# Performance work log

Measured on AMD Instinct MI355X. Metric: run time of the kernel, lower is better.

Reference implementation:

```python
import jax, jax.numpy as jnp
import numpy as np

N_NODES = 40000
N_EDGES = 640000
IN_CH = 128
HID_CH = 128
BN_EPS = 1e-5


def setup_inputs() -> dict:
    key = jax.random.key(0)
    k_x, k_ei, k_w, k_g = jax.random.split(key, 4)
    x = jax.random.normal(k_x, (N_NODES, IN_CH), dtype=jnp.float32)
    edge_index = jax.random.randint(k_ei, (2, N_EDGES), 0, N_NODES, dtype=jnp.int32)
    # Glorot init for GCNConv weight, zero bias (PyG defaults)
    limit = float(np.sqrt(6.0 / (IN_CH + HID_CH)))
    W = jax.random.uniform(k_w, (IN_CH, HID_CH), dtype=jnp.float32, minval=-limit, maxval=limit)
    b = jnp.zeros((HID_CH,), dtype=jnp.float32)
    gamma = jnp.ones((HID_CH,), dtype=jnp.float32)
    beta = jnp.zeros((HID_CH,), dtype=jnp.float32)
    return {"x": x, "edge_index": edge_index, "W": W, "b": b, "gamma": gamma, "beta": beta}


def reference(x, edge_index, W, b, gamma, beta):
    N = x.shape[0]
    src, dst = edge_index[0], edge_index[1]

    # --- GCNConv: h = x @ W, symmetric-normalized aggregation with self-loops ---
    h = x @ W  # [N, H]
    ones = jnp.ones((src.shape[0],), dtype=x.dtype)
    deg = jax.ops.segment_sum(ones, dst, num_segments=N) + 1.0  # +1 for self-loop
    dinv = jax.lax.rsqrt(deg)  # deg >= 1 always
    norm = dinv[src] * dinv[dst]  # [E]
    msg = h[src] * norm[:, None]  # [E, H] gather
    agg = jax.ops.segment_sum(msg, dst, num_segments=N)  # scatter-add
    agg = agg + h * (dinv * dinv)[:, None]  # self-loop contribution
    out = agg + b  # bias added after aggregation (PyG GCNConv)

    # --- BatchNorm1d (training mode: batch stats, biased variance) ---
    mean = jnp.mean(out, axis=0)
    var = jnp.mean((out - mean) ** 2, axis=0)
    out = gamma * (out - mean) * jax.lax.rsqrt(var + BN_EPS) + beta

    # --- ReLU (dropout is a no-op in eval) ---
    return jax.nn.relu(out)
```

## Files before the change

kernel.cpp:

```cpp
#include <hip/hip_runtime.h>

#define N_NODES 40000
#define N_EDGES 640000
#define CH 128
#define BN_EPS 1e-5f
#define CAP 64
#define MM_ROWS 32
#define MM_BLOCKS (N_NODES / MM_ROWS)
#define FILL_BLOCKS ((N_EDGES + 255) / 256)


__device__ __forceinline__ float bf_lo(unsigned u) { return __uint_as_float(u << 16); }
__device__ __forceinline__ float bf_hi(unsigned u) { return __uint_as_float(u & 0xffff0000u); }
__device__ __forceinline__ unsigned short f2bf(float f) {
    unsigned u = __float_as_uint(f);
    unsigned r = 0x7fffu + ((u >> 16) & 1u);
    return (unsigned short)((u + r) >> 16);
}
__device__ __forceinline__ unsigned pack2bf(float a, float b) {
    return (unsigned)f2bf(a) | ((unsigned)f2bf(b) << 16);
}

__global__ __launch_bounds__(256) void mm_fill_kernel(const float* __restrict__ x,
                                                      const float* __restrict__ W,
                                                      unsigned short* __restrict__ hbf,
                                                      const int* __restrict__ src,
                                                      const int* __restrict__ dst,
                                                      int* __restrict__ cnt,
                                                      unsigned short* __restrict__ bucket16) {
    __shared__ unsigned Wsb[CH * CH / 2];
    __shared__ unsigned xsb[CH * 16];
    int t = threadIdx.x;
    int bb = blockIdx.x;
    if (bb % 3 != 0) {
        int fillIdx = bb - (bb / 3) - 1;
        int base = cnt[N_NODES];
        int e = fillIdx * 256 + t;
        if (e < N_EDGES) {
            int d = dst[e];
            int slot = atomicAdd(&cnt[d], 1) - base;
            if (slot < CAP) bucket16[d * CAP + slot] = (unsigned short)src[e];
        }
        return;
    }
    int mmIdx = bb / 3;
    for (int i = t; i < CH * CH / 4; i += 256) {
        float4 w = ((const float4*)W)[i];
        uint2 p;
        p.x = pack2bf(w.x, w.y);
        p.y = pack2bf(w.z, w.w);
        ((uint2*)Wsb)[i] = p;
    }
    size_t row0 = (size_t)mmIdx * MM_ROWS;
    {
        int p = t >> 4;
        int k4a = t & 15;
#pragma unroll
        for (int kk = 0; kk < 2; ++kk) {
            int k4 = k4a + kk * 16;
            float4 xa = ((const float4*)(x + (row0 + p) * CH))[k4];
            float4 xb = ((const float4*)(x + (row0 + p + 16) * CH))[k4];
            xsb[(k4 * 4 + 0) * 16 + p] = pack2bf(xa.x, xb.x);
            xsb[(k4 * 4 + 1) * 16 + p] = pack2bf(xa.y, xb.y);
            xsb[(k4 * 4 + 2) * 16 + p] = pack2bf(xa.z, xb.z);
            xsb[(k4 * 4 + 3) * 16 + p] = pack2bf(xa.w, xb.w);
        }
    }
    __syncthreads();
    int ch4 = t & 31;
    int rg = t >> 5;
    float4 accA = {0,0,0,0}, accB = {0,0,0,0}, accC = {0,0,0,0}, accD = {0,0,0,0};
#pragma unroll 8
    for (int k = 0; k < CH; ++k) {
        uint2 wp = ((const uint2*)Wsb)[k * 32 + ch4];
        unsigned xpa = xsb[k * 16 + rg];
        unsigned xpb = xsb[k * 16 + rg + 8];
        float w0 = bf_lo(wp.x), w1 = bf_hi(wp.x), w2 = bf_lo(wp.y), w3 = bf_hi(wp.y);
        float xa0 = bf_lo(xpa), xa1 = bf_hi(xpa);
        float xb0 = bf_lo(xpb), xb1 = bf_hi(xpb);
        accA.x += xa0 * w0; accA.y += xa0 * w1; accA.z += xa0 * w2; accA.w += xa0 * w3;
        accB.x += xa1 * w0; accB.y += xa1 * w1; accB.z += xa1 * w2; accB.w += xa1 * w3;
        accC.x += xb0 * w0; accC.y += xb0 * w1; accC.z += xb0 * w2; accC.w += xb0 * w3;
        accD.x += xb1 * w0; accD.y += xb1 * w1; accD.z += xb1 * w2; accD.w += xb1 * w3;
    }
    uint2 o;
    o.x = pack2bf(accA.x, accA.y); o.y = pack2bf(accA.z, accA.w);
    ((uint2*)(hbf + (row0 + rg) * CH))[ch4] = o;
    o.x = pack2bf(accB.x, accB.y); o.y = pack2bf(accB.z, accB.w);
    ((uint2*)(hbf + (row0 + rg + 16) * CH))[ch4] = o;
    o.x = pack2bf(accC.x, accC.y); o.y = pack2bf(accC.z, accC.w);
    ((uint2*)(hbf + (row0 + rg + 8) * CH))[ch4] = o;
    o.x = pack2bf(accD.x, accD.y); o.y = pack2bf(accD.z, accD.w);
    ((uint2*)(hbf + (row0 + rg + 24) * CH))[ch4] = o;
}

__global__ __launch_bounds__(256) void aggregate_kernel(const unsigned short* __restrict__ bucket16,
                                                        const int* __restrict__ cnt,
                                                        const unsigned short* __restrict__ hbf,
                                                        const float* __restrict__ b,
                                                        float* __restrict__ out,
                                                        float* __restrict__ sums32) {
    __shared__ float bsum[CH], bsq[CH];
    int t = threadIdx.x;
    if (t < CH) { bsum[t] = 0.0f; bsq[t] = 0.0f; }
    __syncthreads();
    int base = cnt[N_NODES];
    int n = blockIdx.x * 4 + (t >> 6);
    int lane = t & 63;
    int quarter = lane >> 4;
    int ql = lane & 15;
    int cn = cnt[n] - base;
    int m = cn < CAP ? cn : CAP;
    float dn = rsqrtf((float)cn + 1.0f);
    const uint4* h4 = (const uint4*)hbf;
    unsigned sx_pre = (lane < m) ? (unsigned)bucket16[n * CAP + lane] : 0u;
    float a0 = 0, a1 = 0, a2 = 0, a3 = 0, a4 = 0, a5 = 0, a6 = 0, a7 = 0;
    for (int jj = 0; jj < m; jj += 16) {
        int e = jj + quarter * 4;
        unsigned sx0 = (unsigned)__shfl((int)sx_pre, e, 64);
        unsigned sx1 = (unsigned)__shfl((int)sx_pre, e + 1, 64);
        unsigned sx2 = (unsigned)__shfl((int)sx_pre, e + 2, 64);
        unsigned sx3 = (unsigned)__shfl((int)sx_pre, e + 3, 64);
        int c0g = cnt[sx0];
        int c1g = cnt[sx1];
        int c2g = cnt[sx2];
        int c3g = cnt[sx3];
        uint4 r0 = h4[(size_t)sx0 * 16 + ql];
        uint4 r1 = h4[(size_t)sx1 * 16 + ql];
        uint4 r2 = h4[(size_t)sx2 * 16 + ql];
        uint4 r3 = h4[(size_t)sx3 * 16 + ql];
        float d0 = (e     < m) ? rsqrtf((float)(c0g - base) + 1.0f) : 0.0f;
        float d1 = (e + 1 < m) ? rsqrtf((float)(c1g - base) + 1.0f) : 0.0f;
        float d2 = (e + 2 < m) ? rsqrtf((float)(c2g - base) + 1.0f) : 0.0f;
        float d3 = (e + 3 < m) ? rsqrtf((float)(c3g - base) + 1.0f) : 0.0f;
        a0 += bf_lo(r0.x) * d0; a1 += bf_hi(r0.x) * d0;
        a2 += bf_lo(r0.y) * d0; a3 += bf_hi(r0.y) * d0;
        a4 += bf_lo(r0.z) * d0; a5 += bf_hi(r0.z) * d0;
        a6 += bf_lo(r0.w) * d0; a7 += bf_hi(r0.w) * d0;
        a0 += bf_lo(r1.x) * d1; a1 += bf_hi(r1.x) * d1;
        a2 += bf_lo(r1.y) * d1; a3 += bf_hi(r1.y) * d1;
        a4 += bf_lo(r1.z) * d1; a5 += bf_hi(r1.z) * d1;
        a6 += bf_lo(r1.w) * d1; a7 += bf_hi(r1.w) * d1;
        a0 += bf_lo(r2.x) * d2; a1 += bf_hi(r2.x) * d2;
        a2 += bf_lo(r2.y) * d2; a3 += bf_hi(r2.y) * d2;
        a4 += bf_lo(r2.z) * d2; a5 += bf_hi(r2.z) * d2;
        a6 += bf_lo(r2.w) * d2; a7 += bf_hi(r2.w) * d2;
        a0 += bf_lo(r3.x) * d3; a1 += bf_hi(r3.x) * d3;
        a2 += bf_lo(r3.y) * d3; a3 += bf_hi(r3.y) * d3;
        a4 += bf_lo(r3.z) * d3; a5 += bf_hi(r3.z) * d3;
        a6 += bf_lo(r3.w) * d3; a7 += bf_hi(r3.w) * d3;
    }
    a0 += __shfl_xor(a0, 16, 64); a0 += __shfl_xor(a0, 32, 64);
    a1 += __shfl_xor(a1, 16, 64); a1 += __shfl_xor(a1, 32, 64);
    a2 += __shfl_xor(a2, 16, 64); a2 += __shfl_xor(a2, 32, 64);
    a3 += __shfl_xor(a3, 16, 64); a3 += __shfl_xor(a3, 32, 64);
    a4 += __shfl_xor(a4, 16, 64); a4 += __shfl_xor(a4, 32, 64);
    a5 += __shfl_xor(a5, 16, 64); a5 += __shfl_xor(a5, 32, 64);
    a6 += __shfl_xor(a6, 16, 64); a6 += __shfl_xor(a6, 32, 64);
    a7 += __shfl_xor(a7, 16, 64); a7 += __shfl_xor(a7, 32, 64);
    if (quarter == 0) {
        uint4 raw = h4[(size_t)n * 16 + ql];
        float s2 = dn * dn;
        float4 bv0 = ((const float4*)b)[ql * 2];
        float4 bv1 = ((const float4*)b)[ql * 2 + 1];
        float o0 = a0 * dn + bf_lo(raw.x) * s2 + bv0.x;
        float o1 = a1 * dn + bf_hi(raw.x) * s2 + bv0.y;
        float o2 = a2 * dn + bf_lo(raw.y) * s2 + bv0.z;
        float o3 = a3 * dn + bf_hi(raw.y) * s2 + bv0.w;
        float o4 = a4 * dn + bf_lo(raw.z) * s2 + bv1.x;
        float o5 = a5 * dn + bf_hi(raw.z) * s2 + bv1.y;
        float o6 = a6 * dn + bf_lo(raw.w) * s2 + bv1.z;
        float o7 = a7 * dn + bf_hi(raw.w) * s2 + bv1.w;
        float4* op = (float4*)(out + (size_t)n * CH + ql * 8);
        float4 w0 = {o0, o1, o2, o3};
        float4 w1 = {o4, o5, o6, o7};
        op[0] = w0;
        op[1] = w1;
        int c0 = ql * 8;
        atomicAdd(&bsum[c0 + 0], o0); atomicAdd(&bsq[c0 + 0], o0 * o0);
        atomicAdd(&bsum[c0 + 1], o1); atomicAdd(&bsq[c0 + 1], o1 * o1);
        atomicAdd(&bsum[c0 + 2], o2); atomicAdd(&bsq[c0 + 2], o2 * o2);
        atomicAdd(&bsum[c0 + 3], o3); atomicAdd(&bsq[c0 + 3], o3 * o3);
        atomicAdd(&bsum[c0 + 4], o4); atomicAdd(&bsq[c0 + 4], o4 * o4);
        atomicAdd(&bsum[c0 + 5], o5); atomicAdd(&bsq[c0 + 5], o5 * o5);
        atomicAdd(&bsum[c0 + 6], o6); atomicAdd(&bsq[c0 + 6], o6 * o6);
        atomicAdd(&bsum[c0 + 7], o7); atomicAdd(&bsq[c0 + 7], o7 * o7);
    }
    __syncthreads();
    atomicAdd(&sums32[(blockIdx.x & 31) * 256 + t], (t < CH) ? bsum[t] : bsq[t - CH]);
}

__global__ __launch_bounds__(256) void bn_relu_kernel(float* __restrict__ out,
                                                      const float* __restrict__ sums32,
                                                      const float* __restrict__ gamma,
                                                      const float* __restrict__ beta) {
    __shared__ float sc[CH], sh[CH];
    int t = threadIdx.x;
    if (t < CH) {
        float P = sums32[32 * 256];
        float s = -32.0f * P, q = -32.0f * P;
#pragma unroll
        for (int k = 0; k < 32; ++k) {
            s += sums32[k * 256 + t];
            q += sums32[k * 256 + CH + t];
        }
        const float invN = 1.0f / (float)N_NODES;
        float mean = s * invN;
        float var = q * invN - mean * mean;
        float scale = gamma[t] * rsqrtf(var + BN_EPS);
        sc[t] = scale;
        sh[t] = beta[t] - mean * scale;
    }
    __syncthreads();
    int i = blockIdx.x * 256 + t;
    int c0 = (i & 31) * 4;
    float4 v = ((float4*)out)[i];
    float r0 = v.x * sc[c0] + sh[c0];
    float r1 = v.y * sc[c0 + 1] + sh[c0 + 1];
    float r2 = v.z * sc[c0 + 2] + sh[c0 + 2];
    float r3 = v.w * sc[c0 + 3] + sh[c0 + 3];
    v.x = r0 > 0.0f ? r0 : 0.0f;
    v.y = r1 > 0.0f ? r1 : 0.0f;
    v.z = r2 > 0.0f ? r2 : 0.0f;
    v.w = r3 > 0.0f ? r3 : 0.0f;
    ((float4*)out)[i] = v;
}

extern "C" void kernel_launch(void* const* d_in, const int* in_sizes, int n_in,
                              void* d_out, int out_size, void* d_ws, size_t ws_size,
                              hipStream_t stream) {
    const float* x = (const float*)d_in[0];
    const int* ei = (const int*)d_in[1];
    const float* W = (const float*)d_in[2];
    const float* b = (const float*)d_in[3];
    const float* gamma = (const float*)d_in[4];
    const float* beta = (const float*)d_in[5];
    float* out = (float*)d_out;
    const int* src = ei;
    const int* dst = ei + N_EDGES;
    char* ws = (char*)d_ws;

    unsigned short* hbf = (unsigned short*)ws;
    int* cnt = (int*)(ws + 10240000);
    float* sums32 = (float*)(ws + 10400256);
    unsigned short* bucket16 = (unsigned short*)(ws + 10433280);

    mm_fill_kernel<<<MM_BLOCKS + FILL_BLOCKS, 256, 0, stream>>>(x, W, hbf, src, dst, cnt,
                                                                bucket16);
    aggregate_kernel<<<N_NODES / 4, 256, 0, stream>>>(bucket16, cnt, hbf, b, out, sums32);
    bn_relu_kernel<<<N_NODES * CH / 4 / 256, 256, 0, stream>>>(out, sums32, gamma, beta);
}
```

Before: 196.0 us.

## Use bf16 MFMA for the x@W matmul and rebalance fused fill blocks

Replaces the scalar FMA loop in the fused matmul/fill kernel with 16x16x32 bf16 MFMA instructions. W is transposed into padded shared memory and each block now handles 16 rows instead of 32. Fill blocks each process two edges, which changes the interleaving ratio of fill to matmul blocks. This moves the GEMM onto matrix cores to cut ALU time, but each block re-stages all of W for fewer rows. The transposed W store also writes scalar shorts with a strided pattern, which may cause LDS bank conflicts.

New measurement: 201.8 us. 3.0% more time.

```diff
diff --git a/kernel.cpp b/kernel.cpp
--- a/kernel.cpp
+++ b/kernel.cpp
@@ -5,10 +5,14 @@
 #define CH 128
 #define BN_EPS 1e-5f
 #define CAP 64
-#define MM_ROWS 32
+#define MM_ROWS 16
 #define MM_BLOCKS (N_NODES / MM_ROWS)
-#define FILL_BLOCKS ((N_EDGES + 255) / 256)
-
+#define FILL_BLOCKS (N_EDGES / 512)
+#define XPAD 136
+
+
+typedef short short8 __attribute__((ext_vector_type(8)));
+typedef float f32x4 __attribute__((ext_vector_type(4)));
 
 __device__ __forceinline__ float bf_lo(unsigned u) { return __uint_as_float(u << 16); }
 __device__ __forceinline__ float bf_hi(unsigned u) { return __uint_as_float(u & 0xffff0000u); }
@@ -28,70 +32,63 @@
                                                       const int* __restrict__ dst,
                                                       int* __restrict__ cnt,
                                                       unsigned short* __restrict__ bucket16) {
-    __shared__ unsigned Wsb[CH * CH / 2];
-    __shared__ unsigned xsb[CH * 16];
+    __shared__ unsigned short Wt[CH * XPAD];
+    __shared__ unsigned short xs[MM_ROWS * XPAD];
     int t = threadIdx.x;
     int bb = blockIdx.x;
-    if (bb % 3 != 0) {
-        int fillIdx = bb - (bb / 3) - 1;
+    if (bb % 3 == 0) {
+        int fillIdx = bb / 3;
         int base = cnt[N_NODES];
-        int e = fillIdx * 256 + t;
-        if (e < N_EDGES) {
-            int d = dst[e];
-            int slot = atomicAdd(&cnt[d], 1) - base;
-            if (slot < CAP) bucket16[d * CAP + slot] = (unsigned short)src[e];
-        }
+        int e0 = fillIdx * 512 + t;
+        int e1 = e0 + 256;
+        int d0 = dst[e0], d1 = dst[e1];
+        int s0 = src[e0], s1 = src[e1];
+        int slot0 = atomicAdd(&cnt[d0], 1) - base;
+        int slot1 = atomicAdd(&cnt[d1], 1) - base;
+        if (slot0 < CAP) bucket16[d0 * CAP + slot0] = (unsigned short)s0;
+        if (slot1 < CAP) bucket16[d1 * CAP + slot1] = (unsigned short)s1;
         return;
     }
-    int mmIdx = bb / 3;
+    int mmIdx = bb - (bb / 3) - 1;
+    size_t row0 = (size_t)mmIdx * MM_ROWS;
     for (int i = t; i < CH * CH / 4; i += 256) {
         float4 w = ((const float4*)W)[i];
-        uint2 p;
-        p.x = pack2bf(w.x, w.y);
-        p.y = pack2bf(w.z, w.w);
-        ((uint2*)Wsb)[i] = p;
-    }
-    size_t row0 = (size_t)mmIdx * MM_ROWS;
-    {
-        int p = t >> 4;
-        int k4a = t & 15;
-#pragma unroll
-        for (int kk = 0; kk < 2; ++kk) {
-            int k4 = k4a + kk * 16;
-            float4 xa = ((const float4*)(x + (row0 + p) * CH))[k4];
-            float4 xb = ((const float4*)(x + (row0 + p + 16) * CH))[k4];
-            xsb[(k4 * 4 + 0) * 16 + p] = pack2bf(xa.x, xb.x);
-            xsb[(k4 * 4 + 1) * 16 + p] = pack2bf(xa.y, xb.y);
-            xsb[(k4 * 4 + 2) * 16 + p] = pack2bf(xa.z, xb.z);
-            xsb[(k4 * 4 + 3) * 16 + p] = pack2bf(xa.w, xb.w);
+        int k = i >> 5;
+        int c0 = (i & 31) * 4;
+        Wt[(c0 + 0) * XPAD + k] = f2bf(w.x);
+        Wt[(c0 + 1) * XPAD + k] = f2bf(w.y);
+        Wt[(c0 + 2) * XPAD + k] = f2bf(w.z);
+        Wt[(c0 + 3) * XPAD + k] = f2bf(w.w);
+    }
+    for (int i = t; i < MM_ROWS * 32; i += 256) {
+        int r = i >> 5;
+        int c4 = i & 31;
+        float4 xv = ((const float4*)(x + (row0 + r) * CH))[c4];
+        ((unsigned*)xs)[r * (XPAD / 2) + c4 * 2] = pack2bf(xv.x, xv.y);
+        ((unsigned*)xs)[r * (XPAD / 2) + c4 * 2 + 1] = pack2bf(xv.z, xv.w);
+    }
+    __syncthreads();
+    int w = t >> 6;
+    int lane = t & 63;
+    int n = lane & 15;
+    int q = lane >> 4;
+    short8 af[4];
+#pragma unroll
+    for (int kc = 0; kc < 4; ++kc)
+        af[kc] = *(const short8*)(xs + n * XPAD + kc * 32 + q * 8);
+#pragma unroll
+    for (int tt = 0; tt < 2; ++tt) {
+        int c0 = w * 32 + tt * 16;
+        f32x4 acc = {0.0f, 0.0f, 0.0f, 0.0f};
+#pragma unroll
+        for (int kc = 0; kc < 4; ++kc) {
+            short8 bf = *(const short8*)(Wt + (c0 + n) * XPAD + kc * 32 + q * 8);
+            acc = __builtin_amdgcn_mfma_f32_16x16x32_bf16(af[kc], bf, acc, 0, 0, 0);
         }
-    }
-    __syncthreads();
-    int ch4 = t & 31;
-    int rg = t >> 5;
-    float4 accA = {0,0,0,0}, accB = {0,0,0,0}, accC = {0,0,0,0}, accD = {0,0,0,0};
-#pragma unroll 8
-    for (int k = 0; k < CH; ++k) {
-        uint2 wp = ((const uint2*)Wsb)[k * 32 + ch4];
-        unsigned xpa = xsb[k * 16 + rg];
-        unsigned xpb = xsb[k * 16 + rg + 8];
-        float w0 = bf_lo(wp.x), w1 = bf_hi(wp.x), w2 = bf_lo(wp.y), w3 = bf_hi(wp.y);
-        float xa0 = bf_lo(xpa), xa1 = bf_hi(xpa);
-        float xb0 = bf_lo(xpb), xb1 = bf_hi(xpb);
-        accA.x += xa0 * w0; accA.y += xa0 * w1; accA.z += xa0 * w2; accA.w += xa0 * w3;
-        accB.x += xa1 * w0; accB.y += xa1 * w1; accB.z += xa1 * w2; accB.w += xa1 * w3;
-        accC.x += xb0 * w0; accC.y += xb0 * w1; accC.z += xb0 * w2; accC.w += xb0 * w3;
-        accD.x += xb1 * w0; accD.y += xb1 * w1; accD.z += xb1 * w2; accD.w += xb1 * w3;
-    }
-    uint2 o;
-    o.x = pack2bf(accA.x, accA.y); o.y = pack2bf(accA.z, accA.w);
-    ((uint2*)(hbf + (row0 + rg) * CH))[ch4] = o;
-    o.x = pack2bf(accB.x, accB.y); o.y = pack2bf(accB.z, accB.w);
-    ((uint2*)(hbf + (row0 + rg + 16) * CH))[ch4] = o;
-    o.x = pack2bf(accC.x, accC.y); o.y = pack2bf(accC.z, accC.w);
-    ((uint2*)(hbf + (row0 + rg + 8) * CH))[ch4] = o;
-    o.x = pack2bf(accD.x, accD.y); o.y = pack2bf(accD.z, accD.w);
-    ((uint2*)(hbf + (row0 + rg + 24) * CH))[ch4] = o;
+#pragma unroll
+        for (int r = 0; r < 4; ++r)
+            hbf[(row0 + q * 4 + r) * CH + c0 + n] = f2bf(acc[r]);
+    }
 }
 
 __global__ __launch_bounds__(256) void aggregate_kernel(const unsigned short* __restrict__ bucket16,
```
